# Kernel optimization log

Measured on AMD Instinct MI355X. Metric: run time of the kernel, lower is better.

The kernel has to match this reference:

```python
import jax, jax.numpy as jnp
import numpy as np

NUM = 256
T = 0.05
MAXITER = 5


def _constants():
    P = jnp.eye(NUM, dtype=jnp.float32)                  # [num, num]
    Pd = jnp.diff(P, axis=0) / T                          # [num-1, num]
    Pdd = jnp.diff(Pd, axis=0) / T                        # [num-2, num]
    A_eq = P[0:1]                                         # [1, num]
    A_control = jnp.vstack([P, -P, Pd, -Pd, Pdd, -Pdd])   # [6*num-6, num]
    # rho = rho_projection = 1, A_projection = I
    cost = jnp.eye(NUM, dtype=jnp.float32) + A_control.T @ A_control
    cost_mat = jnp.vstack([
        jnp.hstack([cost, A_eq.T]),
        jnp.hstack([A_eq, jnp.zeros((1, 1), dtype=jnp.float32)]),
    ])                                                    # [num+1, num+1]
    return A_eq, A_control, cost_mat


def setup_inputs() -> dict:
    key = jax.random.key(0)
    ks = jax.random.split(key, 8)
    B, IND, H = 4096, 260, 1024
    NC = 6 * NUM - 6
    OUT = NUM + NC
    return {
        "inp": jax.random.normal(ks[0], (B, IND), jnp.float32),
        "steer_init": 0.1 * jax.random.normal(ks[1], (B, 1), jnp.float32),
        "steer_samples": 0.5 * jax.random.normal(ks[2], (B, NUM), jnp.float32),
        "steer_max": jnp.float32(1.0),
        "steer_min": jnp.float32(-1.0),
        "steerdot_max": jnp.float32(2.0),
        "steerdot_min": jnp.float32(-2.0),
        "steerddot_max": jnp.float32(4.0),
        "steerddot_min": jnp.float32(-4.0),
        "median_": jnp.zeros((IND,), jnp.float32),
        "iqr_": jnp.ones((IND,), jnp.float32),
        "W1": 0.02 * jax.random.normal(ks[3], (IND, H), jnp.float32),
        "b1": jnp.zeros((H,), jnp.float32),
        "W2": 0.02 * jax.random.normal(ks[4], (H, OUT), jnp.float32),
        "b2": jnp.zeros((OUT,), jnp.float32),
    }


def reference(inp, steer_init, steer_samples, steer_max, steer_min,
              steerdot_max, steerdot_min, steerddot_max, steerddot_min,
              median_, iqr_, W1, b1, W2, b2):
    A_eq, A_control, cost_mat = _constants()
    B = inp.shape[0]
    NC = A_control.shape[0]
    n1, n2 = NUM - 1, NUM - 2

    # Note: original computes (inp-median)/iqr then overwrites with inp.
    inp_norm = inp
    h = jax.nn.relu(inp_norm @ W1 + b1)
    neural_out = h @ W2 + b2                              # [B, num + nc]
    lamda = neural_out[:, :NUM]
    s = jnp.maximum(0.0, neural_out[:, NUM:NUM + NC])

    b_eq = steer_init * jnp.ones((B, 1), jnp.float32)     # [B, 1]
    ones_n = jnp.ones((B, NUM), jnp.float32)
    ones_n1 = jnp.ones((B, n1), jnp.float32)
    ones_n2 = jnp.ones((B, n2), jnp.float32)
    b_control = jnp.hstack([
        steer_max * ones_n, -steer_min * ones_n,
        steerdot_max * ones_n1, -steerdot_min * ones_n1,
        steerddot_max * ones_n2, -steerddot_min * ones_n2,
    ])                                                    # [B, nc]

    def step(carry, _):
        lamda, s = carry
        b_aug = b_control - s
        # rho = rho_projection = 1, A_projection = I
        lincost = -lamda - steer_samples - b_aug @ A_control   # [B, num]
        rhs = jnp.hstack([-lincost, b_eq])                     # [B, num+1]
        sol = jnp.linalg.solve(cost_mat, rhs.T).T
        steer_proj = sol[:, :NUM]
        As = steer_proj @ A_control.T                          # [B, nc]
        s_new = jnp.maximum(0.0, -As + b_control)
        res_vec = As - b_control + s_new
        res_norm = jnp.linalg.norm(res_vec, axis=1)
        lamda_new = lamda - res_vec @ A_control
        fp = (jnp.linalg.norm(s - s_new, axis=1)
              + jnp.linalg.norm(lamda - lamda_new, axis=1))
        return (lamda_new, s_new), (steer_proj, res_norm, fp)

    (_, _), (projs, prim_stack, fp_stack) = jax.lax.scan(
        step, (lamda, s), None, length=MAXITER)
    steer_projected = projs[-1]
    acc_primal = jnp.sum(prim_stack, axis=0) / MAXITER
    acc_fixed = jnp.sum(fp_stack, axis=0) / MAXITER
    return steer_projected, prim_stack, fp_stack, acc_primal, acc_fixed
```

## Files before the change

### kernel.cpp

```cpp
#include <hip/hip_runtime.h>
#include <cstddef>


#define NUMV 256
#define QP_ITERS 5
#define NO_LD 1792
#define LSCALE 2048.0f
#define INV_LSCALE (1.0f / 2048.0f)

typedef _Float16 f16x4 __attribute__((ext_vector_type(4)));
typedef _Float16 f16x8 __attribute__((ext_vector_type(8)));
typedef float f32x4 __attribute__((ext_vector_type(4)));

struct FacT {
  double invd[256];
  double l1[257];
  double l2[258];
  double z[256];
  float  zcf[256];
};

constexpr double csqrt_(double x) {
  double g = (x > 1.0) ? x : 1.0;
  for (int i = 0; i < 64; ++i) g = 0.5 * (g + x / g);
  return g;
}

constexpr FacT make_fac() {
  FacT f{};
  const double T = 0.05, a = 1.0 / (T * T), b2 = a * a;
  double c0[256] = {}, c1[255] = {}, c2[254] = {};
  double dd[256] = {}, l1[256] = {}, l2[256] = {};
  for (int j = 0; j < 256; j++) {
    double cd1 = (j == 0 || j == 255) ? 1.0 : 2.0;
    double cd2 = (j == 0 || j == 255) ? 1.0 : ((j == 1 || j == 254) ? 5.0 : 6.0);
    c0[j] = 3.0 + 2.0 * a * cd1 + 2.0 * b2 * cd2;
  }
  for (int j = 0; j < 255; j++) c1[j] = -2.0 * a + 2.0 * b2 * ((j == 0 || j == 254) ? -2.0 : -4.0);
  for (int j = 0; j < 254; j++) c2[j] = 2.0 * b2;
  dd[0] = csqrt_(c0[0]); l1[0] = 0.0; l2[0] = 0.0;
  l1[1] = c1[0] / dd[0]; l2[1] = 0.0;
  dd[1] = csqrt_(c0[1] - l1[1] * l1[1]);
  for (int j = 2; j < 256; j++) {
    l2[j] = c2[j - 2] / dd[j - 2];
    l1[j] = (c1[j - 1] - l2[j] * l1[j - 1]) / dd[j - 1];
    dd[j] = csqrt_(c0[j] - l1[j] * l1[j] - l2[j] * l2[j]);
  }
  for (int j = 0; j < 256; j++) f.invd[j] = 1.0 / dd[j];
  for (int j = 0; j < 256; j++) f.l1[j] = l1[j];
  f.l1[256] = 0.0;
  for (int j = 0; j < 256; j++) f.l2[j] = l2[j];
  f.l2[256] = 0.0; f.l2[257] = 0.0;
  double w[256] = {}, zz[256] = {};
  w[0] = 1.0 / dd[0];
  w[1] = (-l1[1] * w[0]) / dd[1];
  for (int j = 2; j < 256; j++) w[j] = (-l1[j] * w[j - 1] - l2[j] * w[j - 2]) / dd[j];
  zz[255] = w[255] / dd[255];
  zz[254] = (w[254] - l1[255] * zz[255]) / dd[254];
  for (int j = 253; j >= 0; j--)
    zz[j] = (w[j] - l1[j + 1] * zz[j + 1] - l2[j + 2] * zz[j + 2]) / dd[j];
  for (int j = 0; j < 256; j++) f.z[j] = zz[j];
  for (int j = 0; j < 256; j++) f.zcf[j] = (float)(zz[j] / zz[0]);
  return f;
}

constexpr FacT FAC_HOST = make_fac();
__constant__ FacT FAC = FAC_HOST;

struct UQ { float u[64][256]; };

constexpr UQ make_uq(int cbase) {
  UQ q{};
  const double T = 0.05, a = 1.0 / (T * T), b2 = a * a;
  double c0a[256] = {}, c1a[255] = {}, c2a[254] = {};
  double dd[256] = {}, l1[256] = {}, l2[256] = {};
  for (int j = 0; j < 256; j++) {
    double cd1 = (j == 0 || j == 255) ? 1.0 : 2.0;
    double cd2 = (j == 0 || j == 255) ? 1.0 : ((j == 1 || j == 254) ? 5.0 : 6.0);
    c0a[j] = 3.0 + 2.0 * a * cd1 + 2.0 * b2 * cd2;
  }
  for (int j = 0; j < 255; j++) c1a[j] = -2.0 * a + 2.0 * b2 * ((j == 0 || j == 254) ? -2.0 : -4.0);
  for (int j = 0; j < 254; j++) c2a[j] = 2.0 * b2;
  dd[0] = csqrt_(c0a[0]); l1[0] = 0.0; l2[0] = 0.0;
  l1[1] = c1a[0] / dd[0]; l2[1] = 0.0;
  dd[1] = csqrt_(c0a[1] - l1[1] * l1[1]);
  for (int j = 2; j < 256; j++) {
    l2[j] = c2a[j - 2] / dd[j - 2];
    l1[j] = (c1a[j - 1] - l2[j] * l1[j - 1]) / dd[j - 1];
    dd[j] = csqrt_(c0a[j] - l1[j] * l1[j] - l2[j] * l2[j]);
  }
  for (int c = cbase; c < cbase + 64; ++c) {
    double w1 = 0.0, w2 = 0.0;
    for (int j = c; j < 256; ++j) {
      const double rhs = (j == c) ? 1.0 : 0.0;
      const double wj = (rhs - l1[j] * w1 - l2[j] * w2) / dd[j];
      q.u[c - cbase][j] = (float)wj;
      w2 = w1; w1 = wj;
    }
  }
  return q;
}

constexpr UQ UQ0_H = make_uq(0);
constexpr UQ UQ1_H = make_uq(64);
constexpr UQ UQ2_H = make_uq(128);
constexpr UQ UQ3_H = make_uq(192);
__constant__ UQ UFQ0 = UQ0_H;
__constant__ UQ UFQ1 = UQ1_H;
__constant__ UQ UFQ2 = UQ2_H;
__constant__ UQ UFQ3 = UQ3_H;

__device__ __forceinline__ const float* uq_row(int c) {
  if (c < 64)  return UFQ0.u[c];
  if (c < 128) return UFQ1.u[c - 64];
  if (c < 192) return UFQ2.u[c - 128];
  return UFQ3.u[c - 192];
}

__device__ __forceinline__ void split8(const float* __restrict__ w, f16x8& h, f16x8& l) {
#pragma unroll
  for (int e = 0; e < 8; e++) {
    const float x = w[e];
    const _Float16 hh = (_Float16)x;
    h[e] = hh;
    l[e] = (_Float16)((x - (float)hh) * LSCALE);
  }
}

__global__ __launch_bounds__(64) void gemm_g(
    _Float16* __restrict__ Gh, _Float16* __restrict__ Gl, float* __restrict__ zc)
{
  const int lane = threadIdx.x;
  const int lr = lane & 15, lg = lane >> 4;
  const int m0 = blockIdx.x * 16, n0 = blockIdx.y * 32;
  if (blockIdx.x == 0 && blockIdx.y == 0) {
    for (int t = lane; t < 256; t += 64) zc[t] = FAC.zcf[t];
  }
  f32x4 accH[2], accL[2];
#pragma unroll
  for (int nf = 0; nf < 2; nf++) { accH[nf] = (f32x4)0.0f; accL[nf] = (f32x4)0.0f; }
  const float* arow = uq_row(m0 + lr);
  const float* brow0 = uq_row(n0 + lr);
  const float* brow1 = uq_row(n0 + 16 + lr);
#pragma unroll 2
  for (int k0 = 0; k0 < 256; k0 += 32) {
    f16x8 ah, al;
    split8(arow + k0 + lg * 8, ah, al);
#pragma unroll
    for (int nf = 0; nf < 2; nf++) {
      f16x8 bh, bl;
      split8((nf ? brow1 : brow0) + k0 + lg * 8, bh, bl);
      accH[nf] = __builtin_amdgcn_mfma_f32_16x16x32_f16(ah, bh, accH[nf], 0, 0, 0);
      accL[nf] = __builtin_amdgcn_mfma_f32_16x16x32_f16(ah, bl, accL[nf], 0, 0, 0);
      accL[nf] = __builtin_amdgcn_mfma_f32_16x16x32_f16(al, bh, accL[nf], 0, 0, 0);
    }
  }
  const int row0 = m0 + lg * 4;
#pragma unroll
  for (int nf = 0; nf < 2; nf++) {
    const int col = n0 + nf * 16 + lr;
    const double zcd = FAC.z[col] / FAC.z[0];
#pragma unroll
    for (int r = 0; r < 4; r++) {
      const int row = row0 + r;
      const float g = accH[nf][r] + accL[nf][r] * INV_LSCALE
                    - (float)(FAC.z[row] * zcd);
      const _Float16 gh = (_Float16)g;
      Gh[(size_t)row * 256 + col] = gh;
      Gl[(size_t)row * 256 + col] = (_Float16)((g - (float)gh) * LSCALE);
    }
  }
}

__global__ __launch_bounds__(256) void transpose_cvt(
    const float* __restrict__ in, _Float16* __restrict__ out, int K, int N, int KP)
{
  __shared__ float t[32][33];
  const int bk = blockIdx.x * 32, bn = blockIdx.y * 32;
  const int x = threadIdx.x, y = threadIdx.y;
  for (int yy = y; yy < 32; yy += 8) {
    const int k = bk + yy, n = bn + x;
    t[yy][x] = (k < K && n < N) ? in[(size_t)k * N + n] : 0.f;
  }
  __syncthreads();
  for (int yy = y; yy < 32; yy += 8) {
    const int n = bn + yy, k = bk + x;
    if (n < N && k < KP) out[(size_t)n * KP + k] = (_Float16)t[x][yy];
  }
}

template<bool A_FP32, bool OUT_H16>
__global__ __launch_bounds__(256) void mfma_gemm(
    const void* __restrict__ Av, const _Float16* __restrict__ Bt,
    const float* __restrict__ bias, void* __restrict__ Cv,
    int M, int Nv, int K, int lda, int ldk, int ldc)
{
  __shared__ _Float16 At[128][40];
  __shared__ _Float16 Bs[128][32];
  const int tid = threadIdx.x;
  const int lane = tid & 63, wid = tid >> 6;
  const int wr = wid >> 1, wc = wid & 1;
  const int lrow = lane & 15, lb = lane >> 4;
  const int m0 = blockIdx.x * 128, n0 = blockIdx.y * 128;
  const int srow = tid >> 1, skh = (tid & 1) * 16;

  const int rl4 = lane >> 2;
  const int kswz = 8 * ((lane & 3) ^ (rl4 & 3));

  f32x4 acc[4][4];
#pragma unroll
  for (int i = 0; i < 4; i++)
#pragma unroll
    for (int j = 0; j < 4; j++) acc[i][j] = (f32x4)0.0f;

  const int nsteps = (K + 31) / 32;
  for (int t = 0; t < nsteps; ++t) {
    const int k0 = t * 32;
    if (A_FP32) {
      const float* A = (const float*)Av;
#pragma unroll
      for (int i = 0; i < 4; i++) {
        const int k = k0 + skh + i * 4;
        f16x4 hv = {};
        if (k + 4 <= K) {
          const float4 v = *reinterpret_cast<const float4*>(&A[(size_t)(m0 + srow) * lda + k]);
          hv[0] = (_Float16)v.x; hv[1] = (_Float16)v.y;
          hv[2] = (_Float16)v.z; hv[3] = (_Float16)v.w;
        } else if (k < K) {
          for (int e = 0; e < 4; e++)
            if (k + e < K) hv[e] = (_Float16)A[(size_t)(m0 + srow) * lda + k + e];
        }
        *reinterpret_cast<f16x4*>(&At[srow][skh + i * 4]) = hv;
      }
    } else {
      const _Float16* A = (const _Float16*)Av;
#pragma unroll
      for (int i = 0; i < 4; i++) {
        const int k = k0 + skh + i * 4;
        f16x4 hv = {};
        if (k + 4 <= K) hv = *reinterpret_cast<const f16x4*>(&A[(size_t)(m0 + srow) * lda + k]);
        *reinterpret_cast<f16x4*>(&At[srow][skh + i * 4]) = hv;
      }
    }
    {
#pragma unroll
      for (int c = 0; c < 2; ++c) {
        const int ci = wid * 2 + c;
        const _Float16* bsrc = &Bt[(size_t)(n0 + ci * 16 + rl4) * ldk + k0 + kswz];
        __builtin_amdgcn_global_load_lds(
            (const __attribute__((address_space(1))) void*)bsrc,
            (__attribute__((address_space(3))) void*)(&Bs[ci * 16][0]), 16, 0, 0);
      }
    }
    __syncthreads();
    f16x8 af[4], bf[4];
#pragma unroll
    for (int i = 0; i < 4; i++)
      af[i] = *reinterpret_cast<const f16x8*>(&At[wr * 64 + i * 16 + lrow][lb * 8]);
#pragma unroll
    for (int j = 0; j < 4; j++) {
      const int r = wc * 64 + j * 16 + lrow;
      bf[j] = *reinterpret_cast<const f16x8*>(&Bs[r][(lb * 8) ^ ((r & 3) << 3)]);
    }
#pragma unroll
    for (int i = 0; i < 4; i++)
#pragma unroll
      for (int j = 0; j < 4; j++)
        acc[i][j] = __builtin_amdgcn_mfma_f32_16x16x32_f16(af[i], bf[j], acc[i][j], 0, 0, 0);
    __syncthreads();
  }
#pragma unroll
  for (int i = 0; i < 4; i++) {
#pragma unroll
    for (int j = 0; j < 4; j++) {
      const int gcol = n0 + wc * 64 + j * 16 + lrow;
      if (gcol < Nv) {
        const float bv = bias[gcol];
#pragma unroll
        for (int r = 0; r < 4; r++) {
          const int grow = m0 + wr * 64 + i * 16 + lb * 4 + r;
          float v = acc[i][j][r] + bv;
          if (OUT_H16) {
            v = fmaxf(v, 0.f);
            ((_Float16*)Cv)[(size_t)grow * ldc + gcol] = (_Float16)v;
          } else {
            ((float*)Cv)[(size_t)grow * ldc + gcol] = v;
          }
        }
      }
    }
  }
}

__global__ __launch_bounds__(256) void mfma_gemm64(
    const _Float16* __restrict__ A, const _Float16* __restrict__ Bt,
    const float* __restrict__ bias, float* __restrict__ C,
    int M, int Nv, int K, int lda, int ldk, int ldc)
{
  __shared__ _Float16 At[128][64];
  __shared__ _Float16 Bs[128][64];
  const int tid = threadIdx.x;
  const int lane = tid & 63, wid = tid >> 6;
  const int wr = wid >> 1, wc = wid & 1;
  const int lrow = lane & 15, lb = lane >> 4;
  const int m0 = blockIdx.x * 128, n0 = blockIdx.y * 128;

  const int srow8 = lane >> 3;
  const int kswz = 8 * ((lane & 7) ^ srow8);

  f32x4 acc[4][4];
#pragma unroll
  for (int i = 0; i < 4; i++)
#pragma unroll
    for (int j = 0; j < 4; j++) acc[i][j] = (f32x4)0.0f;

  const int nsteps = K >> 6;
  for (int t = 0; t < nsteps; ++t) {
    const int k0 = t * 64;
#pragma unroll
    for (int c = 0; c < 4; ++c) {
      const int ci = wid * 4 + c;
      const int row = ci * 8 + srow8;
      const _Float16* asrc = &A[(size_t)(m0 + row) * lda + k0 + kswz];
      const _Float16* bsrc = &Bt[(size_t)(n0 + row) * ldk + k0 + kswz];
      __builtin_amdgcn_global_load_lds(
          (const __attribute__((address_space(1))) void*)asrc,
          (__attribute__((address_space(3))) void*)(&At[ci * 8][0]), 16, 0, 0);
      __builtin_amdgcn_global_load_lds(
          (const __attribute__((address_space(1))) void*)bsrc,
          (__attribute__((address_space(3))) void*)(&Bs[ci * 8][0]), 16, 0, 0);
    }
    __syncthreads();
#pragma unroll
    for (int h = 0; h < 2; h++) {
      f16x8 af[4], bf[4];
#pragma unroll
      for (int i = 0; i < 4; i++) {
        const int r = wr * 64 + i * 16 + lrow;
        af[i] = *reinterpret_cast<const f16x8*>(
            &At[r][(h * 32 + lb * 8) ^ ((r & 7) << 3)]);
      }
#pragma unroll
      for (int j = 0; j < 4; j++) {
        const int r = wc * 64 + j * 16 + lrow;
        bf[j] = *reinterpret_cast<const f16x8*>(
            &Bs[r][(h * 32 + lb * 8) ^ ((r & 7) << 3)]);
      }
#pragma unroll
      for (int i = 0; i < 4; i++)
#pragma unroll
        for (int j = 0; j < 4; j++)
          acc[i][j] = __builtin_amdgcn_mfma_f32_16x16x32_f16(af[i], bf[j], acc[i][j], 0, 0, 0);
    }
    __syncthreads();
  }
#pragma unroll
  for (int i = 0; i < 4; i++) {
#pragma unroll
    for (int j = 0; j < 4; j++) {
      const int gcol = n0 + wc * 64 + j * 16 + lrow;
      if (gcol < Nv) {
        const float bv = bias[gcol];
#pragma unroll
        for (int r = 0; r < 4; r++) {
          const int grow = m0 + wr * 64 + i * 16 + lb * 4 + r;
          C[(size_t)grow * ldc + gcol] = acc[i][j][r] + bv;
        }
      }
    }
  }
}

__global__ __launch_bounds__(1024) void qp_solve5(
    const _Float16* __restrict__ Gh, const _Float16* __restrict__ Gl,
    const float* __restrict__ beq, const float* __restrict__ zc,
    const float* __restrict__ NO, const float* __restrict__ ss,
    const float* __restrict__ p_smax, const float* __restrict__ p_smin,
    const float* __restrict__ p_sdmax, const float* __restrict__ p_sdmin,
    const float* __restrict__ p_sddmax, const float* __restrict__ p_sddmin,
    float* __restrict__ out, int B)
{
  __shared__ float xsA[16][264], xsB[16][264];
  __shared__ _Float16 vhs[16][264], vls[16][264];
  __shared__ float zcs[256], beqs[16];
  __shared__ float red[16][4][3];
  const int tid = threadIdx.x;
  const int wave = tid >> 6, lane = tid & 63;
  const int lr = lane & 15, lg = lane >> 4;
  const int m0 = blockIdx.x * 16;
  const int n0 = wave * 16;
  const int j = tid & 255, half = tid >> 8;

  const float smax = *p_smax, smin = *p_smin;
  const float sdmax = *p_sdmax, sdmin = *p_sdmin;
  const float sddmax = *p_sddmax, sddmin = *p_sddmin;
  const float K0 = smax + smin, K1 = sdmax + sdmin, K2 = sddmax + sddmin;
  const float invT = 20.f, invT2 = 400.f;
  const bool h1 = j < 255, h2 = j < 254;

  f16x8 gh_r[8];
#pragma unroll
  for (int kk = 0; kk < 8; kk++) {
    const size_t bidx = (size_t)(n0 + lr) * 256 + kk * 32 + lg * 8;
    gh_r[kk] = *reinterpret_cast<const f16x8*>(&Gh[bidx]);
  }

  float lamr[4], ssv[4];
#pragma unroll
  for (int rr = 0; rr < 4; rr++) {
    const int rl = half * 4 + rr;
    const int gr = m0 + rl;
    const float* no = NO + (size_t)gr * NO_LD;
    ssv[rr] = ss[(size_t)gr * NUMV + j];
    lamr[rr] = no[j];
    const float D0 = K0 - fmaxf(0.f, no[256 + j]) + fmaxf(0.f, no[512 + j]);
    const float D1j = h1 ? (K1 - fmaxf(0.f, no[768 + j]) + fmaxf(0.f, no[1023 + j])) : 0.f;
    const float D1m = (j >= 1) ? (K1 - fmaxf(0.f, no[768 + j - 1]) + fmaxf(0.f, no[1023 + j - 1])) : 0.f;
    const float D2j = h2 ? (K2 - fmaxf(0.f, no[1278 + j]) + fmaxf(0.f, no[1532 + j])) : 0.f;
    const float D2m1 = (j >= 1 && h1) ? (K2 - fmaxf(0.f, no[1278 + j - 1]) + fmaxf(0.f, no[1532 + j - 1])) : 0.f;
    const float D2m2 = (j >= 2) ? (K2 - fmaxf(0.f, no[1278 + j - 2]) + fmaxf(0.f, no[1532 + j - 2])) : 0.f;
    const float vn = lamr[rr] + ssv[rr]
                   + D0 + (D1m - D1j) * invT + (D2m2 - 2.f * D2m1 + D2j) * invT2;
    const _Float16 vh16 = (_Float16)vn;
    vhs[rl][j] = vh16;
    vls[rl][j] = (_Float16)((vn - (float)vh16) * LSCALE);
  }
  if (tid < 256) zcs[tid] = zc[tid];
  if (tid < 16) {
    beqs[tid] = beq[m0 + tid];
    xsA[tid][0] = 0.f; xsA[tid][1] = 0.f; xsA[tid][258] = 0.f; xsA[tid][259] = 0.f;
    xsB[tid][0] = 0.f; xsB[tid][1] = 0.f; xsB[tid][258] = 0.f; xsB[tid][259] = 0.f;
  }
  float accP = 0.f, accF = 0.f;

  const size_t primOff = (size_t)B * NUMV;
  const size_t fpOff = primOff + (size_t)QP_ITERS * B;
  const size_t accPOff = fpOff + (size_t)QP_ITERS * B;
  const size_t accFOff = accPOff + (size_t)B;

  float (*xc)[264] = xsA;
  float (*xp)[264] = xsB;

  __syncthreads();

  for (int it = 0; it < QP_ITERS; ++it) {
    f32x4 accH = (f32x4)0.0f, accL = (f32x4)0.0f;
#pragma unroll
    for (int kk = 0; kk < 8; kk++) {
      const f16x8 ah = *reinterpret_cast<const f16x8*>(&vhs[lr][kk * 32 + lg * 8]);
      const f16x8 al = *reinterpret_cast<const f16x8*>(&vls[lr][kk * 32 + lg * 8]);
      const f16x8 bl = *reinterpret_cast<const f16x8*>(
          &Gl[(size_t)(n0 + lr) * 256 + kk * 32 + lg * 8]);
      accH = __builtin_amdgcn_mfma_f32_16x16x32_f16(ah, gh_r[kk], accH, 0, 0, 0);
      accL = __builtin_amdgcn_mfma_f32_16x16x32_f16(ah, bl, accL, 0, 0, 0);
      accL = __builtin_amdgcn_mfma_f32_16x16x32_f16(al, gh_r[kk], accL, 0, 0, 0);
    }
    {
      const int r0l = lg * 4;
      const int col = n0 + lr;
      const float zv = zcs[col];
#pragma unroll
      for (int r = 0; r < 4; r++)
        xc[r0l + r][col + 2] = accH[r] + accL[r] * INV_LSCALE + beqs[r0l + r] * zv;
    }
    __syncthreads();

#pragma unroll
    for (int rr = 0; rr < 4; rr++) {
      const int rl = half * 4 + rr;
      const int gr = m0 + rl;
      const float xm2 = xc[rl][j];
      const float xm1 = xc[rl][j + 1];
      const float x0  = xc[rl][j + 2];
      const float x1  = xc[rl][j + 3];
      const float x2  = xc[rl][j + 4];

      const float vj = (x1 - x0) * invT;
      const float aj = (x2 - 2.f * x1 + x0) * invT2;
      const float vm1 = (x0 - xm1) * invT;
      const float am1 = (x1 - 2.f * x0 + xm1) * invT2;
      const float am2 = (x0 - 2.f * xm1 + xm2) * invT2;

      const float rv0a = fmaxf(0.f, x0 - smax), rv0b = fmaxf(0.f, smin - x0);
      const float E0 = rv0a - rv0b;
      float rv1a = 0.f, rv1b = 0.f, rv2a = 0.f, rv2b = 0.f, E1 = 0.f, E2 = 0.f;
      if (h1) { rv1a = fmaxf(0.f, vj - sdmax); rv1b = fmaxf(0.f, sdmin - vj); E1 = rv1a - rv1b; }
      if (h2) { rv2a = fmaxf(0.f, aj - sddmax); rv2b = fmaxf(0.f, sddmin - aj); E2 = rv2a - rv2b; }
      float res2 = rv0a * rv0a + rv0b * rv0b + rv1a * rv1a + rv1b * rv1b
                 + rv2a * rv2a + rv2b * rv2b;

      const float E1m = (j >= 1) ? (fmaxf(0.f, vm1 - sdmax) - fmaxf(0.f, sdmin - vm1)) : 0.f;
      const float E2m1 = (j >= 1 && h1) ? (fmaxf(0.f, am1 - sddmax) - fmaxf(0.f, sddmin - am1)) : 0.f;
      const float E2m2 = (j >= 2) ? (fmaxf(0.f, am2 - sddmax) - fmaxf(0.f, sddmin - am2)) : 0.f;

      const float dl = E0 + (E1m - E1) * invT + (E2m2 - 2.f * E2m1 + E2) * invT2;
      const float lnew = lamr[rr] - dl;
      const float fpl2 = dl * dl;
      lamr[rr] = lnew;

      const float sn0a = fmaxf(0.f, smax - x0), sn0b = fmaxf(0.f, x0 - smin);
      float sn1a = 0.f, sn1b = 0.f, sn2a = 0.f, sn2b = 0.f;
      if (h1) { sn1a = fmaxf(0.f, sdmax - vj); sn1b = fmaxf(0.f, vj - sdmin); }
      if (h2) { sn2a = fmaxf(0.f, sddmax - aj); sn2b = fmaxf(0.f, aj - sddmin); }

      float sp0a, sp0b, sp1a = 0.f, sp1b = 0.f, sp2a = 0.f, sp2b = 0.f;
      if (it == 0) {
        const float* no = NO + (size_t)gr * NO_LD;
        sp0a = fmaxf(0.f, no[256 + j]); sp0b = fmaxf(0.f, no[512 + j]);
        if (h1) { sp1a = fmaxf(0.f, no[768 + j]); sp1b = fmaxf(0.f, no[1023 + j]); }
        if (h2) { sp2a = fmaxf(0.f, no[1278 + j]); sp2b = fmaxf(0.f, no[1532 + j]); }
      } else {
        const float p0 = xp[rl][j + 2], p1 = xp[rl][j + 3], p2 = xp[rl][j + 4];
        const float vp = (p1 - p0) * invT;
        const float ap = (p2 - 2.f * p1 + p0) * invT2;
        sp0a = fmaxf(0.f, smax - p0); sp0b = fmaxf(0.f, p0 - smin);
        if (h1) { sp1a = fmaxf(0.f, sdmax - vp); sp1b = fmaxf(0.f, vp - sdmin); }
        if (h2) { sp2a = fmaxf(0.f, sddmax - ap); sp2b = fmaxf(0.f, ap - sddmin); }
      }
      const float d0a = sp0a - sn0a, d0b = sp0b - sn0b;
      const float d1a = sp1a - sn1a, d1b = sp1b - sn1b;
      const float d2a = sp2a - sn2a, d2b = sp2b - sn2b;
      float fps2 = d0a * d0a + d0b * d0b + d1a * d1a + d1b * d1b
                 + d2a * d2a + d2b * d2b;

      const float D0 = fminf(smax, x0) + fmaxf(smin, x0);
      const float D1 = h1 ? (fminf(sdmax, vj) + fmaxf(sdmin, vj)) : 0.f;
      const float D2 = h2 ? (fminf(sddmax, aj) + fmaxf(sddmin, aj)) : 0.f;
      const float D1m = (j >= 1) ? (fminf(sdmax, vm1) + fmaxf(sdmin, vm1)) : 0.f;
      const float D2m1 = (j >= 1 && h1) ? (fminf(sddmax, am1) + fmaxf(sddmin, am1)) : 0.f;
      const float D2m2 = (j >= 2) ? (fminf(sddmax, am2) + fmaxf(sddmin, am2)) : 0.f;

      if (it < QP_ITERS - 1) {
        const float vn = lnew + ssv[rr]
                       + D0 + (D1m - D1) * invT + (D2m2 - 2.f * D2m1 + D2) * invT2;
        const _Float16 vh16 = (_Float16)vn;
        vhs[rl][j] = vh16;
        vls[rl][j] = (_Float16)((vn - (float)vh16) * LSCALE);
      } else {
        out[(size_t)gr * NUMV + j] = x0;
      }

      float a = res2, b = fps2, c = fpl2;
      for (int o = 32; o > 0; o >>= 1) {
        a += __shfl_down(a, o);
        b += __shfl_down(b, o);
        c += __shfl_down(c, o);
      }
      if (lane == 0) { red[wave][rr][0] = a; red[wave][rr][1] = b; red[wave][rr][2] = c; }
    }
    __syncthreads();

    if (tid < 16) {
      const int rl = tid, hf = rl >> 2, rr = rl & 3;
      const int w0 = hf * 4;
      const float r2 = red[w0][rr][0] + red[w0 + 1][rr][0] + red[w0 + 2][rr][0] + red[w0 + 3][rr][0];
      const float s2 = red[w0][rr][1] + red[w0 + 1][rr][1] + red[w0 + 2][rr][1] + red[w0 + 3][rr][1];
      const float l2 = red[w0][rr][2] + red[w0 + 1][rr][2] + red[w0 + 2][rr][2] + red[w0 + 3][rr][2];
      const float pr = sqrtf(r2);
      const float fp = sqrtf(s2) + sqrtf(l2);
      out[primOff + (size_t)it * B + m0 + rl] = pr;
      out[fpOff + (size_t)it * B + m0 + rl] = fp;
      accP += pr; accF += fp;
    }
    float (*t)[264] = xc; xc = xp; xp = t;
  }
  if (tid < 16) {
    out[accPOff + m0 + tid] = accP * (1.f / QP_ITERS);
    out[accFOff + m0 + tid] = accF * (1.f / QP_ITERS);
  }
}

extern "C" void kernel_launch(void* const* d_in, const int* in_sizes, int n_in,
                              void* d_out, int out_size, void* d_ws, size_t ws_size,
                              hipStream_t stream)
{
  const float* inp = (const float*)d_in[0];
  const float* sinit = (const float*)d_in[1];
  const float* ssamp = (const float*)d_in[2];
  const float* p_smax = (const float*)d_in[3];
  const float* p_smin = (const float*)d_in[4];
  const float* p_sdmax = (const float*)d_in[5];
  const float* p_sdmin = (const float*)d_in[6];
  const float* p_sddmax = (const float*)d_in[7];
  const float* p_sddmin = (const float*)d_in[8];
  const float* W1 = (const float*)d_in[11];
  const float* b1 = (const float*)d_in[12];
  const float* W2 = (const float*)d_in[13];
  const float* b2 = (const float*)d_in[14];
  float* out = (float*)d_out;

  const int B = in_sizes[1];
  const int IND = in_sizes[9];
  const int H = in_sizes[12];
  const int OUTN = in_sizes[14];
  const int KP1 = 288;

  char* ws = (char*)d_ws;
  float* NO = (float*)ws;
  char* p = ws + (size_t)B * NO_LD * 4;
  _Float16* hH = (_Float16*)p;
  char* q = p + (size_t)B * H * 2;
  _Float16* W2T = (_Float16*)q;
  char* q2 = q + (size_t)OUTN * H * 2;
  _Float16* W1T = (_Float16*)q2;
  char* r4 = ws + 46137344;
  _Float16* Gh = (_Float16*)r4;
  _Float16* Gl = (_Float16*)(r4 + 131072);
  float* zc = (float*)(r4 + 262144);

  {
    dim3 g(16, 8);
    gemm_g<<<g, 64, 0, stream>>>(Gh, Gl, zc);
  }
  {
    dim3 g((KP1 + 31) / 32, (H + 31) / 32), blk(32, 8);
    transpose_cvt<<<g, blk, 0, stream>>>(W1, W1T, IND, H, KP1);
  }
  {
    dim3 g((H + 31) / 32, (OUTN + 31) / 32), blk(32, 8);
    transpose_cvt<<<g, blk, 0, stream>>>(W2, W2T, H, OUTN, H);
  }
  {
    dim3 g(B / 128, H / 128);
    mfma_gemm<true, true><<<g, 256, 0, stream>>>(inp, W1T, b1, hH, B, H, IND, IND, KP1, H);
  }
  {
    dim3 g(B / 128, (OUTN + 127) / 128);
    mfma_gemm64<<<g, 256, 0, stream>>>(hH, W2T, b2, NO, B, OUTN, H, H, H, NO_LD);
  }
  qp_solve5<<<B / 16, 1024, 0, stream>>>(Gh, Gl, sinit, zc, NO, ssamp,
                                         p_smax, p_smin, p_sdmax, p_sdmin,
                                         p_sddmax, p_sddmin, out, B);
}
```

Before: 135.4 us.

## Merge prep kernels into one launch and pre-convert input to padded fp16

Folds the G-matrix build, the two weight transposes and a new fp32-to-fp16 padded conversion of the input into a single block-indexed prep kernel, cutting three launches down to one. The first GEMM now reads the pre-converted fp16 input through direct global-to-LDS loads with a swizzle, the same way B was already loaded, instead of converting fp32 in registers. The aim is less launch overhead and a faster GEMM inner loop. The cost is an extra fp16 copy of the input in workspace and a dependence on hardcoded sizes (1024 hidden, 288 padded K, 4096 rows).

Measured after the change: 119.2 us. 1.14x faster.

```diff
diff --git a/kernel.cpp b/kernel.cpp
--- a/kernel.cpp
+++ b/kernel.cpp
@@ -127,13 +127,13 @@
   }
 }
 
-__global__ __launch_bounds__(64) void gemm_g(
-    _Float16* __restrict__ Gh, _Float16* __restrict__ Gl, float* __restrict__ zc)
+__device__ void gemm_g_body(
+    _Float16* __restrict__ Gh, _Float16* __restrict__ Gl, float* __restrict__ zc,
+    int gx, int gy, int lane)
 {
-  const int lane = threadIdx.x;
   const int lr = lane & 15, lg = lane >> 4;
-  const int m0 = blockIdx.x * 16, n0 = blockIdx.y * 32;
-  if (blockIdx.x == 0 && blockIdx.y == 0) {
+  const int m0 = gx * 16, n0 = gy * 32;
+  if (gx == 0 && gy == 0) {
     for (int t = lane; t < 256; t += 64) zc[t] = FAC.zcf[t];
   }
   f32x4 accH[2], accL[2];
@@ -172,12 +172,13 @@
   }
 }
 
-__global__ __launch_bounds__(256) void transpose_cvt(
-    const float* __restrict__ in, _Float16* __restrict__ out, int K, int N, int KP)
+__device__ void transpose_body(
+    const float* __restrict__ in, _Float16* __restrict__ out,
+    int K, int N, int KP, int bx, int by, int tid)
 {
   __shared__ float t[32][33];
-  const int bk = blockIdx.x * 32, bn = blockIdx.y * 32;
-  const int x = threadIdx.x, y = threadIdx.y;
+  const int bk = bx * 32, bn = by * 32;
+  const int x = tid & 31, y = tid >> 5;
   for (int yy = y; yy < 32; yy += 8) {
     const int k = bk + yy, n = bn + x;
     t[yy][x] = (k < K && n < N) ? in[(size_t)k * N + n] : 0.f;
@@ -189,21 +190,49 @@
   }
 }
 
-template<bool A_FP32, bool OUT_H16>
-__global__ __launch_bounds__(256) void mfma_gemm(
-    const void* __restrict__ Av, const _Float16* __restrict__ Bt,
-    const float* __restrict__ bias, void* __restrict__ Cv,
-    int M, int Nv, int K, int lda, int ldk, int ldc)
+#define PREP_G   128
+#define PREP_T1  288
+#define PREP_T2  1792
+#define PREP_CV  256
+__global__ __launch_bounds__(256) void prep(
+    _Float16* __restrict__ Gh, _Float16* __restrict__ Gl, float* __restrict__ zc,
+    const float* __restrict__ W1, _Float16* __restrict__ W1T,
+    const float* __restrict__ W2, _Float16* __restrict__ W2T,
+    const float* __restrict__ inp, _Float16* __restrict__ hA,
+    int IND, int OUTN)
 {
-  __shared__ _Float16 At[128][40];
+  const int bid = blockIdx.x;
+  const int tid = threadIdx.x;
+  if (bid < PREP_G) {
+    if (tid < 64) gemm_g_body(Gh, Gl, zc, bid & 15, bid >> 4, tid);
+  } else if (bid < PREP_G + PREP_T1) {
+    const int i = bid - PREP_G;
+    transpose_body(W1, W1T, IND, 1024, 288, i % 9, i / 9, tid);
+  } else if (bid < PREP_G + PREP_T1 + PREP_T2) {
+    const int i = bid - PREP_G - PREP_T1;
+    transpose_body(W2, W2T, 1024, OUTN, 1024, i & 31, i >> 5, tid);
+  } else {
+    const int r0 = (bid - PREP_G - PREP_T1 - PREP_T2) * 16;
+    for (int idx = tid; idx < 16 * 288; idx += 256) {
+      const int r = r0 + idx / 288, c = idx % 288;
+      hA[(size_t)r * 288 + c] =
+          (c < IND) ? (_Float16)inp[(size_t)r * IND + c] : (_Float16)0.f;
+    }
+  }
+}
+
+__global__ __launch_bounds__(256) void mfma_gemm32(
+    const _Float16* __restrict__ A, const _Float16* __restrict__ Bt,
+    const float* __restrict__ bias, _Float16* __restrict__ C,
+    int KP, int ldc)
+{
+  __shared__ _Float16 At[128][32];
   __shared__ _Float16 Bs[128][32];
   const int tid = threadIdx.x;
   const int lane = tid & 63, wid = tid >> 6;
   const int wr = wid >> 1, wc = wid & 1;
   const int lrow = lane & 15, lb = lane >> 4;
   const int m0 = blockIdx.x * 128, n0 = blockIdx.y * 128;
-  const int srow = tid >> 1, skh = (tid & 1) * 16;
-
   const int rl4 = lane >> 2;
   const int kswz = 8 * ((lane & 3) ^ (rl4 & 3));
 
@@ -213,50 +242,28 @@
 #pragma unroll
     for (int j = 0; j < 4; j++) acc[i][j] = (f32x4)0.0f;
 
-  const int nsteps = (K + 31) / 32;
+  const int nsteps = KP >> 5;
   for (int t = 0; t < nsteps; ++t) {
     const int k0 = t * 32;
-    if (A_FP32) {
-      const float* A = (const float*)Av;
-#pragma unroll
-      for (int i = 0; i < 4; i++) {
-        const int k = k0 + skh + i * 4;
-        f16x4 hv = {};
-        if (k + 4 <= K) {
-          const float4 v = *reinterpret_cast<const float4*>(&A[(size_t)(m0 + srow) * lda + k]);
-          hv[0] = (_Float16)v.x; hv[1] = (_Float16)v.y;
-          hv[2] = (_Float16)v.z; hv[3] = (_Float16)v.w;
-        } else if (k < K) {
-          for (int e = 0; e < 4; e++)
-            if (k + e < K) hv[e] = (_Float16)A[(size_t)(m0 + srow) * lda + k + e];
-        }
-        *reinterpret_cast<f16x4*>(&At[srow][skh + i * 4]) = hv;
-      }
-    } else {
-      const _Float16* A = (const _Float16*)Av;
-#pragma unroll
-      for (int i = 0; i < 4; i++) {
-        const int k = k0 + skh + i * 4;
-        f16x4 hv = {};
-        if (k + 4 <= K) hv = *reinterpret_cast<const f16x4*>(&A[(size_t)(m0 + srow) * lda + k]);
-        *reinterpret_cast<f16x4*>(&At[srow][skh + i * 4]) = hv;
-      }
-    }
-    {
-#pragma unroll
-      for (int c = 0; c < 2; ++c) {
-        const int ci = wid * 2 + c;
-        const _Float16* bsrc = &Bt[(size_t)(n0 + ci * 16 + rl4) * ldk + k0 + kswz];
-        __builtin_amdgcn_global_load_lds(
-            (const __attribute__((address_space(1))) void*)bsrc,
-            (__attribute__((address_space(3))) void*)(&Bs[ci * 16][0]), 16, 0, 0);
-      }
+#pragma unroll
+    for (int c = 0; c < 2; ++c) {
+      const int ci = wid * 2 + c;
+      const _Float16* asrc = &A[(size_t)(m0 + ci * 16 + rl4) * KP + k0 + kswz];
+      const _Float16* bsrc = &Bt[(size_t)(n0 + ci * 16 + rl4) * KP + k0 + kswz];
+      __builtin_amdgcn_global_load_lds(
+          (const __attribute__((address_space(1))) void*)asrc,
+          (__attribute__((address_space(3))) void*)(&At[ci * 16][0]), 16, 0, 0);
+      __builtin_amdgcn_global_load_lds(
+          (const __attribute__((address_space(1))) void*)bsrc,
+          (__attribute__((address_space(3))) void*)(&Bs[ci * 16][0]), 16, 0, 0);
     }
     __syncthreads();
     f16x8 af[4], bf[4];
 #pragma unroll
-    for (int i = 0; i < 4; i++)
-      af[i] = *reinterpret_cast<const f16x8*>(&At[wr * 64 + i * 16 + lrow][lb * 8]);
+    for (int i = 0; i < 4; i++) {
+      const int r = wr * 64 + i * 16 + lrow;
+      af[i] = *reinterpret_cast<const f16x8*>(&At[r][(lb * 8) ^ ((r & 3) << 3)]);
+    }
 #pragma unroll
     for (int j = 0; j < 4; j++) {
       const int r = wc * 64 + j * 16 + lrow;
@@ -274,19 +281,12 @@
 #pragma unroll
     for (int j = 0; j < 4; j++) {
       const int gcol = n0 + wc * 64 + j * 16 + lrow;
-      if (gcol < Nv) {
-        const float bv = bias[gcol];
-#pragma unroll
-        for (int r = 0; r < 4; r++) {
-          const int grow = m0 + wr * 64 + i * 16 + lb * 4 + r;
-          float v = acc[i][j][r] + bv;
-          if (OUT_H16) {
-            v = fmaxf(v, 0.f);
-            ((_Float16*)Cv)[(size_t)grow * ldc + gcol] = (_Float16)v;
-          } else {
-            ((float*)Cv)[(size_t)grow * ldc + gcol] = v;
-          }
-        }
+      const float bv = bias[gcol];
+#pragma unroll
+      for (int r = 0; r < 4; r++) {
+        const int grow = m0 + wr * 64 + i * 16 + lb * 4 + r;
+        const float v = fmaxf(acc[i][j][r] + bv, 0.f);
+        C[(size_t)grow * ldc + gcol] = (_Float16)v;
       }
     }
   }
@@ -603,26 +603,17 @@
   _Float16* W2T = (_Float16*)q;
   char* q2 = q + (size_t)OUTN * H * 2;
   _Float16* W1T = (_Float16*)q2;
+  _Float16* hA = (_Float16*)(q2 + (size_t)H * KP1 * 2);
   char* r4 = ws + 46137344;
   _Float16* Gh = (_Float16*)r4;
   _Float16* Gl = (_Float16*)(r4 + 131072);
   float* zc = (float*)(r4 + 262144);
 
-  {
-    dim3 g(16, 8);
-    gemm_g<<<g, 64, 0, stream>>>(Gh, Gl, zc);
-  }
-  {
-    dim3 g((KP1 + 31) / 32, (H + 31) / 32), blk(32, 8);
-    transpose_cvt<<<g, blk, 0, stream>>>(W1, W1T, IND, H, KP1);
-  }
-  {
-    dim3 g((H + 31) / 32, (OUTN + 31) / 32), blk(32, 8);
-    transpose_cvt<<<g, blk, 0, stream>>>(W2, W2T, H, OUTN, H);
-  }
+  prep<<<PREP_G + PREP_T1 + PREP_T2 + PREP_CV, 256, 0, stream>>>(
+      Gh, Gl, zc, W1, W1T, W2, W2T, inp, hA, IND, OUTN);
   {
     dim3 g(B / 128, H / 128);
-    mfma_gemm<true, true><<<g, 256, 0, stream>>>(inp, W1T, b1, hH, B, H, IND, IND, KP1, H);
+    mfma_gemm32<<<g, 256, 0, stream>>>(hA, W1T, b1, hH, KP1, H);
   }
   {
     dim3 g(B / 128, (OUTN + 127) / 128);
```
